# Optimization experiments

Measured on AMD Instinct MI355X. Metric: run time of the kernel, lower is better.

## Reference

```python
import jax, jax.numpy as jnp
import numpy as np

B, N, D_IN, D_OUT, HEADS = 4, 4096, 1024, 1024, 16
D_HEAD = D_OUT // HEADS  # scale_factor in the torch module


def setup_inputs() -> dict:
    key = jax.random.key(0)
    ks = jax.random.split(key, 5)
    x = jax.random.normal(ks[0], (B, N, D_IN), dtype=jnp.float32)
    s_in = 1.0 / np.sqrt(D_IN)
    s_out = 1.0 / np.sqrt(D_OUT)
    Wq = jax.random.normal(ks[1], (D_IN, D_OUT), dtype=jnp.float32) * s_in
    Wk = jax.random.normal(ks[2], (D_IN, D_OUT), dtype=jnp.float32) * s_in
    Wv = jax.random.normal(ks[3], (D_IN, D_OUT), dtype=jnp.float32) * s_in
    Wo = jax.random.normal(ks[4], (D_OUT, D_OUT), dtype=jnp.float32) * s_out
    bo = jnp.zeros((D_OUT,), dtype=jnp.float32)
    return {"x": x, "Wq": Wq, "Wk": Wk, "Wv": Wv, "Wo": Wo, "bo": bo}


def reference(x, Wq, Wk, Wv, Wo, bo):
    # Linear attention (Efficient Attention): softmax(Q, feat) @ (softmax(K, seq)^T @ V)
    q = jax.nn.softmax(jnp.einsum('bni,io->bno', x, Wq), axis=-1)   # [B,N,D] softmax over features
    k = jax.nn.softmax(jnp.einsum('bni,io->bno', x, Wk), axis=-2)   # [B,N,D] softmax over sequence
    v = jnp.einsum('bni,io->bno', x, Wv)                             # [B,N,D]
    scale = 1.0 / np.sqrt(D_HEAD).astype(np.float32)
    # context = K^T V : [B, D, D] -- avoids the [B, N, N] score matrix
    ctx = jnp.einsum('bnd,bne->bde', k, v) * scale
    y = jnp.einsum('bnd,bde->bne', q, ctx) / jnp.float32(D_OUT)      # final per-elem / shape[-1]
    # dropout is identity in eval mode
    return jnp.einsum('bnd,de->bne', y, Wo) + bo
```

## Files before the change

### kernel.cpp

```cpp
#include <hip/hip_runtime.h>

typedef _Float16 half_t;
typedef __attribute__((ext_vector_type(8))) _Float16 half8;
typedef __attribute__((ext_vector_type(4))) _Float16 half4;
typedef __attribute__((ext_vector_type(4))) float f32x4;

#define B_ 4
#define N_ 4096
#define D_ 1024
#define R_ (B_ * N_)

__device__ __forceinline__ void gload_lds16(const half_t* g, half_t* l) {
    __builtin_amdgcn_global_load_lds(
        (const __attribute__((address_space(1))) unsigned int*)g,
        (__attribute__((address_space(3))) unsigned int*)l, 16, 0, 0);
}

__device__ __forceinline__ void wgbar() {
    asm volatile("" ::: "memory");
    __builtin_amdgcn_s_barrier();
    asm volatile("" ::: "memory");
}

template <int EPI, int ZSHIFT, int SWAP>
__global__ __launch_bounds__(512, 2) void gemm256(
    const half_t* __restrict__ A, const half_t* __restrict__ Bt,
    void* __restrict__ Cv, const float* __restrict__ bias,
    int lda, int ldb, int ldc, int K,
    long sA, long sB, long sC, float scale)
{
    __shared__ __align__(16) half_t As[2][2][256 * 32];
    __shared__ __align__(16) half_t Bs[2][2][256 * 32];

    const int t = threadIdx.x;
    const int wave = t >> 6;
    const int lane = t & 63;
    const int l15 = lane & 15;
    const int q = lane >> 4;
    const int wm = wave >> 2;
    const int wn = wave & 3;
    const int m0 = (SWAP ? blockIdx.x : blockIdx.y) * 256;
    const int n0 = (SWAP ? blockIdx.y : blockIdx.x) * 256;
    const long zb = blockIdx.z >> ZSHIFT;
    const int zs = blockIdx.z & ((1 << ZSHIFT) - 1);

    const int c0 = t, c1 = t + 512;
    const int r0 = c0 >> 2, r1 = c1 >> 2;
    const int g0 = ((c0 & 3) ^ ((c0 >> 3) & 3)) * 8;
    const int g1 = ((c1 & 3) ^ ((c1 >> 3) & 3)) * 8;

    const half_t* Ab = A + zb * sA + (long)m0 * lda + zs * K;
    const half_t* Bb = Bt + zb * sB + (long)n0 * ldb + zs * K;
    const long a0 = (long)r0 * lda + g0, a1 = (long)r1 * lda + g1;
    const long b0 = (long)r0 * ldb + g0, b1 = (long)r1 * ldb + g1;

    const int qq = (q ^ ((l15 >> 1) & 3)) * 8;

    f32x4 acc[8][4] = {};
    const int nk2 = K >> 6;

#define STAGE_A(tt, ks) do { const int kb_ = (tt) * 64 + (ks) * 32; \
        gload_lds16(Ab + a0 + kb_, &As[(tt) & 1][ks][c0 * 8]);      \
        gload_lds16(Ab + a1 + kb_, &As[(tt) & 1][ks][c1 * 8]); } while (0)
#define STAGE_B(tt, ks) do { const int kb_ = (tt) * 64 + (ks) * 32; \
        gload_lds16(Bb + b0 + kb_, &Bs[(tt) & 1][ks][c0 * 8]);      \
        gload_lds16(Bb + b1 + kb_, &Bs[(tt) & 1][ks][c1 * 8]); } while (0)
#define LDB4(ksb) _Pragma("unroll") \
    for (int j = 0; j < 4; j++)     \
        bf[j] = *(const half8*)&Bs[cur][ksb][(wn * 64 + j * 16 + l15) * 32 + qq];
#define LDA4(ksb, mh) _Pragma("unroll") \
    for (int i = 0; i < 4; i++)         \
        af[i] = *(const half8*)&As[cur][ksb][(wm * 128 + (mh) * 64 + i * 16 + l15) * 32 + qq];
#define MFMA16(ar) _Pragma("unroll")                    \
    for (int i = 0; i < 4; i++) _Pragma("unroll")       \
        for (int j = 0; j < 4; j++)                     \
            acc[(ar) + i][j] = __builtin_amdgcn_mfma_f32_16x16x32_f16(af[i], bf[j], acc[(ar) + i][j], 0, 0, 0);

    STAGE_A(0, 0); STAGE_B(0, 0); STAGE_A(0, 1); STAGE_B(0, 1);
    if (nk2 > 1) {
        STAGE_A(1, 0); STAGE_B(1, 0); STAGE_B(1, 1);
        asm volatile("s_waitcnt vmcnt(6)" ::: "memory");
    } else {
        asm volatile("s_waitcnt vmcnt(0)" ::: "memory");
    }
    wgbar();

    for (int tt = 0; tt < nk2; ++tt) {
        const int cur = tt & 1;
        half8 af[4], bf[4];
        LDB4(0); LDA4(0, 0);
        if (tt + 1 < nk2) STAGE_A(tt + 1, 1);
        wgbar();
        __builtin_amdgcn_s_setprio(1); MFMA16(0); __builtin_amdgcn_s_setprio(0);
        wgbar();
        LDA4(0, 1);
        if (tt + 2 < nk2) STAGE_B(tt + 2, 0);
        wgbar();
        __builtin_amdgcn_s_setprio(1); MFMA16(4); __builtin_amdgcn_s_setprio(0);
        wgbar();
        LDB4(1); LDA4(1, 0);
        if (tt + 2 < nk2) STAGE_A(tt + 2, 0);
        wgbar();
        __builtin_amdgcn_s_setprio(1); MFMA16(0); __builtin_amdgcn_s_setprio(0);
        wgbar();
        LDA4(1, 1);
        if (tt + 2 < nk2) STAGE_B(tt + 2, 1);
        wgbar();
        __builtin_amdgcn_s_setprio(1); MFMA16(4); __builtin_amdgcn_s_setprio(0);
        if (tt + 2 < nk2) asm volatile("s_waitcnt vmcnt(6)" ::: "memory");
        else              asm volatile("s_waitcnt vmcnt(0)" ::: "memory");
        wgbar();
    }
#undef STAGE_A
#undef STAGE_B
#undef LDB4
#undef LDA4
#undef MFMA16

    if (EPI == 1) {
        half_t* C = (half_t*)Cv + (long)blockIdx.z * sC + (long)m0 * ldc + n0;
#pragma unroll
        for (int a = 0; a < 8; a++) {
            const int rowb = wm * 128 + (a >> 2) * 64 + (a & 3) * 16 + q * 4;
#pragma unroll
            for (int j = 0; j < 4; j++) {
                const int col = wn * 64 + j * 16 + l15;
#pragma unroll
                for (int r = 0; r < 4; r++)
                    C[(long)(rowb + r) * ldc + col] = (half_t)(acc[a][j][r] * scale);
            }
        }
    } else {
        float* C = (float*)Cv + (long)blockIdx.z * sC + (long)m0 * ldc + n0;
#pragma unroll
        for (int a = 0; a < 8; a++) {
            const int rowb = wm * 128 + (a >> 2) * 64 + (a & 3) * 16 + q * 4;
#pragma unroll
            for (int j = 0; j < 4; j++) {
                const int col = wn * 64 + j * 16 + l15;
                const float bv = (EPI == 2) ? bias[n0 + col] : 0.0f;
#pragma unroll
                for (int r = 0; r < 4; r++)
                    C[(long)(rowb + r) * ldc + col] = acc[a][j][r] * scale + bv;
            }
        }
    }
}

__global__ __launch_bounds__(256) void ctx_reduce_h(
    const half_t* __restrict__ P, half_t* __restrict__ ctx)
{
    const long i = ((long)blockIdx.x * 256 + threadIdx.x) * 8;
    const long b = i >> 20;
    const long idx = i & ((1L << 20) - 1);
    const half_t* p = P + (b * 4) * (1L << 20) + idx;
    const half8 s0 = *(const half8*)(p);
    const half8 s1 = *(const half8*)(p + (1L << 20));
    const half8 s2 = *(const half8*)(p + 2 * (1L << 20));
    const half8 s3 = *(const half8*)(p + 3 * (1L << 20));
    half8 o;
#pragma unroll
    for (int j = 0; j < 8; j++)
        o[j] = (half_t)((float)s0[j] + (float)s1[j] + (float)s2[j] + (float)s3[j]);
    *(half8*)(ctx + i) = o;
}

__global__ __launch_bounds__(256) void convert_f32_f16(
    const float* __restrict__ in, half_t* __restrict__ out)
{
    const long i = ((long)blockIdx.x * 256 + threadIdx.x) * 8;
    const float4 a = *(const float4*)(in + i);
    const float4 b = *(const float4*)(in + i + 4);
    half8 o = {(half_t)a.x, (half_t)a.y, (half_t)a.z, (half_t)a.w,
               (half_t)b.x, (half_t)b.y, (half_t)b.z, (half_t)b.w};
    *(half8*)(out + i) = o;
}

__global__ void transpose_w4(const float* __restrict__ W0, const float* __restrict__ W1,
                             const float* __restrict__ W2, const float* __restrict__ W3,
                             half_t* __restrict__ Wt)
{
    __shared__ float tile[32][33];
    const float* W = blockIdx.z == 0 ? W0 : blockIdx.z == 1 ? W1
                   : blockIdx.z == 2 ? W2 : W3;
    half_t* dst = Wt + (size_t)blockIdx.z * 1024 * 1024;
    const int tx = threadIdx.x, ty = threadIdx.y;
    const int bx = blockIdx.x * 32, by = blockIdx.y * 32;
#pragma unroll
    for (int yy = ty; yy < 32; yy += 8)
        tile[yy][tx] = W[(long)(by + yy) * 1024 + bx + tx];
    __syncthreads();
#pragma unroll
    for (int yy = ty; yy < 32; yy += 8)
        dst[(long)(bx + yy) * 1024 + by + tx] = (half_t)tile[tx][yy];
}

__global__ __launch_bounds__(256) void softmax_rows(
    const half_t* __restrict__ L, half_t* __restrict__ Qh)
{
    const int r = blockIdx.x;
    const int t = threadIdx.x;
    const half4 xh = ((const half4*)(L + (long)r * 1024))[t];
    const float x0 = (float)xh[0], x1 = (float)xh[1],
                x2 = (float)xh[2], x3 = (float)xh[3];
    float m = fmaxf(fmaxf(x0, x1), fmaxf(x2, x3));
#pragma unroll
    for (int o = 32; o > 0; o >>= 1) m = fmaxf(m, __shfl_xor(m, o, 64));
    __shared__ float redm[4], reds[4];
    const int wave = t >> 6;
    if ((t & 63) == 0) redm[wave] = m;
    __syncthreads();
    m = fmaxf(fmaxf(redm[0], redm[1]), fmaxf(redm[2], redm[3]));
    const float e0 = __expf(x0 - m), e1 = __expf(x1 - m),
                e2 = __expf(x2 - m), e3 = __expf(x3 - m);
    float s = e0 + e1 + e2 + e3;
#pragma unroll
    for (int o = 32; o > 0; o >>= 1) s += __shfl_xor(s, o, 64);
    if ((t & 63) == 0) reds[wave] = s;
    __syncthreads();
    s = reds[0] + reds[1] + reds[2] + reds[3];
    const float rs = 64.0f / s;
    half4 o4 = {(half_t)(e0 * rs), (half_t)(e1 * rs),
                (half_t)(e2 * rs), (half_t)(e3 * rs)};
    ((half4*)(Qh + (long)r * 1024))[t] = o4;
}

__global__ __launch_bounds__(256) void softmax_seq(
    const half_t* __restrict__ L, half_t* __restrict__ O)
{
    const long r = blockIdx.x;
    const int t = threadIdx.x;
    const half_t* row = L + r * 4096;
    const half8 h0 = *(const half8*)(row + t * 16);
    const half8 h1 = *(const half8*)(row + t * 16 + 8);
    float v[16];
#pragma unroll
    for (int j = 0; j < 8; j++) { v[j] = (float)h0[j]; v[8 + j] = (float)h1[j]; }
    float m = v[0];
#pragma unroll
    for (int j = 1; j < 16; j++) m = fmaxf(m, v[j]);
#pragma unroll
    for (int o = 32; o > 0; o >>= 1) m = fmaxf(m, __shfl_xor(m, o, 64));
    __shared__ float redm[4], reds[4];
    const int wave = t >> 6;
    if ((t & 63) == 0) redm[wave] = m;
    __syncthreads();
    m = fmaxf(fmaxf(redm[0], redm[1]), fmaxf(redm[2], redm[3]));
    float s = 0.0f;
#pragma unroll
    for (int j = 0; j < 16; j++) { v[j] = __expf(v[j] - m); s += v[j]; }
#pragma unroll
    for (int o = 32; o > 0; o >>= 1) s += __shfl_xor(s, o, 64);
    if ((t & 63) == 0) reds[wave] = s;
    __syncthreads();
    s = reds[0] + reds[1] + reds[2] + reds[3];
    const float rs = 64.0f / s;
    half8 o0, o1;
#pragma unroll
    for (int j = 0; j < 8; j++) {
        o0[j] = (half_t)(v[j] * rs);
        o1[j] = (half_t)(v[8 + j] * rs);
    }
    *(half8*)(O + r * 4096 + t * 16) = o0;
    *(half8*)(O + r * 4096 + t * 16 + 8) = o1;
}

extern "C" void kernel_launch(void* const* d_in, const int* in_sizes, int n_in,
                              void* d_out, int out_size, void* d_ws, size_t ws_size,
                              hipStream_t stream)
{
    const float* x  = (const float*)d_in[0];
    const float* Wq = (const float*)d_in[1];
    const float* Wk = (const float*)d_in[2];
    const float* Wv = (const float*)d_in[3];
    const float* Wo = (const float*)d_in[4];
    const float* bo = (const float*)d_in[5];
    float* out = (float*)d_out;

    char* w = (char*)d_ws;
    half_t* Xh  = (half_t*)w;
    half_t* P   = (half_t*)w;
    half_t* L   = (half_t*)(w + ((size_t)R_ * D_ * 2));
    w += (size_t)R_ * D_ * 4;
    half_t* Qh  = (half_t*)w; w += (size_t)R_ * D_ * 2;
    half_t* Kt  = (half_t*)w; w += (size_t)R_ * D_ * 2;
    half_t* Vt  = (half_t*)w; w += (size_t)R_ * D_ * 2;
    half_t* Wt  = (half_t*)w; w += (size_t)4 * D_ * D_ * 2;
    half_t* ctx = (half_t*)w; w += (size_t)B_ * D_ * D_ * 2;
    half_t* Mt  = (half_t*)w; w += (size_t)B_ * D_ * D_ * 2;
    (void)ws_size; (void)in_sizes; (void)n_in; (void)out_size;

    const dim3 blk(256);
    const dim3 blkg(512);
    const long M1 = 1L << 20;

    convert_f32_f16<<<R_ * D_ / (256 * 8), blk, 0, stream>>>(x, Xh);
    transpose_w4<<<dim3(32, 32, 4), dim3(32, 8), 0, stream>>>(Wq, Wk, Wv, Wo, Wt);

    gemm256<1, 0, 1><<<dim3(64, 4, 1), blkg, 0, stream>>>(Xh, Wt, L, nullptr,
        1024, 1024, 1024, 1024, 0, 0, 0, 1.0f);
    softmax_rows<<<R_, blk, 0, stream>>>(L, Qh);

    gemm256<1, 0, 0><<<dim3(16, 4, B_), blkg, 0, stream>>>(Wt + M1, Xh, L, nullptr,
        1024, 1024, 4096, 1024, 0, (long)N_ * D_, (long)D_ * N_, 1.0f);
    softmax_seq<<<B_ * D_, blk, 0, stream>>>(L, Kt);

    gemm256<1, 0, 0><<<dim3(16, 4, B_), blkg, 0, stream>>>(Wt + 2 * M1, Xh, Vt, nullptr,
        1024, 1024, 4096, 1024, 0, (long)N_ * D_, (long)D_ * N_, 1.0f);

    gemm256<1, 2, 1><<<dim3(4, 4, 16), blkg, 0, stream>>>(Kt, Vt, P, nullptr,
        N_, N_, 1024, N_ / 4,
        (long)D_ * N_, (long)D_ * N_, M1, 1.0f);
    ctx_reduce_h<<<2048, blk, 0, stream>>>(P, ctx);

    gemm256<1, 2, 1><<<dim3(4, 4, 16), blkg, 0, stream>>>(Wt + 3 * M1, ctx, P, nullptr,
        1024, 1024, 1024, 256,
        0, M1, M1, 1.0f);
    ctx_reduce_h<<<2048, blk, 0, stream>>>(P, Mt);

    gemm256<2, 0, 1><<<dim3(16, 4, B_), blkg, 0, stream>>>(Qh, Mt, out, bo,
        1024, 1024, 1024, 1024,
        (long)N_ * D_, M1, (long)N_ * D_,
        1.0f / 33554432.0f);
}
```

Before: 389.2 us.

## Simplify GEMM pipeline to 4-buffer K32 stages and fuse K/V projection GEMMs

The GEMM main loop changes from a two-half-K, four-barrier-per-iteration schedule to a simpler four-slot ring of 32-wide K tiles. Two tiles are prefetched ahead, with one barrier per step and all 32 MFMAs issued together. Separately, the K and V projections become one launch with doubled grid height, writing into an interleaved K/V region that softmax_seq and the ctx GEMM index with new strides. This removes a launch and gives more blocks per wave, but the coarser schedule may overlap LDS reads and MFMA less well and raises register pressure (af[8]).

```diff
diff --git a/kernel.cpp b/kernel.cpp
--- a/kernel.cpp
+++ b/kernel.cpp
@@ -29,8 +29,8 @@
     int lda, int ldb, int ldc, int K,
     long sA, long sB, long sC, float scale)
 {
-    __shared__ __align__(16) half_t As[2][2][256 * 32];
-    __shared__ __align__(16) half_t Bs[2][2][256 * 32];
+    __shared__ __align__(16) half_t As[4][256 * 32];
+    __shared__ __align__(16) half_t Bs[4][256 * 32];
 
     const int t = threadIdx.x;
     const int wave = t >> 6;
@@ -57,91 +57,66 @@
     const int qq = (q ^ ((l15 >> 1) & 3)) * 8;
 
     f32x4 acc[8][4] = {};
-    const int nk2 = K >> 6;
-
-#define STAGE_A(tt, ks) do { const int kb_ = (tt) * 64 + (ks) * 32; \
-        gload_lds16(Ab + a0 + kb_, &As[(tt) & 1][ks][c0 * 8]);      \
-        gload_lds16(Ab + a1 + kb_, &As[(tt) & 1][ks][c1 * 8]); } while (0)
-#define STAGE_B(tt, ks) do { const int kb_ = (tt) * 64 + (ks) * 32; \
-        gload_lds16(Bb + b0 + kb_, &Bs[(tt) & 1][ks][c0 * 8]);      \
-        gload_lds16(Bb + b1 + kb_, &Bs[(tt) & 1][ks][c1 * 8]); } while (0)
-#define LDB4(ksb) _Pragma("unroll") \
-    for (int j = 0; j < 4; j++)     \
-        bf[j] = *(const half8*)&Bs[cur][ksb][(wn * 64 + j * 16 + l15) * 32 + qq];
-#define LDA4(ksb, mh) _Pragma("unroll") \
-    for (int i = 0; i < 4; i++)         \
-        af[i] = *(const half8*)&As[cur][ksb][(wm * 128 + (mh) * 64 + i * 16 + l15) * 32 + qq];
-#define MFMA16(ar) _Pragma("unroll")                    \
-    for (int i = 0; i < 4; i++) _Pragma("unroll")       \
-        for (int j = 0; j < 4; j++)                     \
-            acc[(ar) + i][j] = __builtin_amdgcn_mfma_f32_16x16x32_f16(af[i], bf[j], acc[(ar) + i][j], 0, 0, 0);
-
-    STAGE_A(0, 0); STAGE_B(0, 0); STAGE_A(0, 1); STAGE_B(0, 1);
-    if (nk2 > 1) {
-        STAGE_A(1, 0); STAGE_B(1, 0); STAGE_B(1, 1);
-        asm volatile("s_waitcnt vmcnt(6)" ::: "memory");
-    } else {
-        asm volatile("s_waitcnt vmcnt(0)" ::: "memory");
+    const int nk = K >> 5;
+
+#define STAGE(kt) do { const int kb_ = (kt) * 32; const int bf_ = (kt) & 3; \
+        gload_lds16(Ab + a0 + kb_, &As[bf_][c0 * 8]);                       \
+        gload_lds16(Ab + a1 + kb_, &As[bf_][c1 * 8]);                       \
+        gload_lds16(Bb + b0 + kb_, &Bs[bf_][c0 * 8]);                       \
+        gload_lds16(Bb + b1 + kb_, &Bs[bf_][c1 * 8]); } while (0)
+
+    STAGE(0); STAGE(1);
+    asm volatile("s_waitcnt vmcnt(4)" ::: "memory");
+    wgbar();
+
+    for (int kt = 0; kt < nk; ++kt) {
+        const int cb = kt & 3;
+        if (kt + 2 < nk) STAGE(kt + 2);
+        half8 bf[4], af[8];
+#pragma unroll
+        for (int j = 0; j < 4; j++)
+            bf[j] = *(const half8*)&Bs[cb][(wn * 64 + j * 16 + l15) * 32 + qq];
+#pragma unroll
+        for (int i = 0; i < 8; i++)
+            af[i] = *(const half8*)&As[cb][(wm * 128 + i * 16 + l15) * 32 + qq];
+        __builtin_amdgcn_s_setprio(1);
+#pragma unroll
+        for (int i = 0; i < 8; i++)
+#pragma unroll
+            for (int j = 0; j < 4; j++)
+                acc[i][j] = __builtin_amdgcn_mfma_f32_16x16x32_f16(af[i], bf[j], acc[i][j], 0, 0, 0);
+        __builtin_amdgcn_s_setprio(0);
+        if (kt + 2 < nk)      asm volatile("s_waitcnt vmcnt(4)" ::: "memory");
+        else if (kt + 1 < nk) asm volatile("s_waitcnt vmcnt(0)" ::: "memory");
+        if (kt + 1 < nk) wgbar();
     }
-    wgbar();
-
-    for (int tt = 0; tt < nk2; ++tt) {
-        const int cur = tt & 1;
-        half8 af[4], bf[4];
-        LDB4(0); LDA4(0, 0);
-        if (tt + 1 < nk2) STAGE_A(tt + 1, 1);
-        wgbar();
-        __builtin_amdgcn_s_setprio(1); MFMA16(0); __builtin_amdgcn_s_setprio(0);
-        wgbar();
-        LDA4(0, 1);
-        if (tt + 2 < nk2) STAGE_B(tt + 2, 0);
-        wgbar();
-        __builtin_amdgcn_s_setprio(1); MFMA16(4); __builtin_amdgcn_s_setprio(0);
-        wgbar();
-        LDB4(1); LDA4(1, 0);
-        if (tt + 2 < nk2) STAGE_A(tt + 2, 0);
-        wgbar();
-        __builtin_amdgcn_s_setprio(1); MFMA16(0); __builtin_amdgcn_s_setprio(0);
-        wgbar();
-        LDA4(1, 1);
-        if (tt + 2 < nk2) STAGE_B(tt + 2, 1);
-        wgbar();
-        __builtin_amdgcn_s_setprio(1); MFMA16(4); __builtin_amdgcn_s_setprio(0);
-        if (tt + 2 < nk2) asm volatile("s_waitcnt vmcnt(6)" ::: "memory");
-        else              asm volatile("s_waitcnt vmcnt(0)" ::: "memory");
-        wgbar();
-    }
-#undef STAGE_A
-#undef STAGE_B
-#undef LDB4
-#undef LDA4
-#undef MFMA16
+#undef STAGE
 
     if (EPI == 1) {
         half_t* C = (half_t*)Cv + (long)blockIdx.z * sC + (long)m0 * ldc + n0;
 #pragma unroll
-        for (int a = 0; a < 8; a++) {
-            const int rowb = wm * 128 + (a >> 2) * 64 + (a & 3) * 16 + q * 4;
+        for (int i = 0; i < 8; i++) {
+            const int rowb = wm * 128 + i * 16 + q * 4;
 #pragma unroll
             for (int j = 0; j < 4; j++) {
                 const int col = wn * 64 + j * 16 + l15;
 #pragma unroll
                 for (int r = 0; r < 4; r++)
-                    C[(long)(rowb + r) * ldc + col] = (half_t)(acc[a][j][r] * scale);
+                    C[(long)(rowb + r) * ldc + col] = (half_t)(acc[i][j][r] * scale);
             }
         }
     } else {
         float* C = (float*)Cv + (long)blockIdx.z * sC + (long)m0 * ldc + n0;
 #pragma unroll
-        for (int a = 0; a < 8; a++) {
-            const int rowb = wm * 128 + (a >> 2) * 64 + (a & 3) * 16 + q * 4;
+        for (int i = 0; i < 8; i++) {
+            const int rowb = wm * 128 + i * 16 + q * 4;
 #pragma unroll
             for (int j = 0; j < 4; j++) {
                 const int col = wn * 64 + j * 16 + l15;
                 const float bv = (EPI == 2) ? bias[n0 + col] : 0.0f;
 #pragma unroll
                 for (int r = 0; r < 4; r++)
-                    C[(long)(rowb + r) * ldc + col] = acc[a][j][r] * scale + bv;
+                    C[(long)(rowb + r) * ldc + col] = acc[i][j][r] * scale + bv;
             }
         }
     }
@@ -226,11 +201,13 @@
 }
 
 __global__ __launch_bounds__(256) void softmax_seq(
-    const half_t* __restrict__ L, half_t* __restrict__ O)
+    const half_t* __restrict__ KV, half_t* __restrict__ O)
 {
     const long r = blockIdx.x;
+    const long b = r >> 10;
+    const long d = r & 1023;
     const int t = threadIdx.x;
-    const half_t* row = L + r * 4096;
+    const half_t* row = KV + (b * 2048 + d) * 4096;
     const half8 h0 = *(const half8*)(row + t * 16);
     const half8 h1 = *(const half8*)(row + t * 16 + 8);
     float v[16];
@@ -280,11 +257,12 @@
     char* w = (char*)d_ws;
     half_t* Xh  = (half_t*)w;
     half_t* P   = (half_t*)w;
-    half_t* L   = (half_t*)(w + ((size_t)R_ * D_ * 2));
-    w += (size_t)R_ * D_ * 4;
+    w += (size_t)R_ * D_ * 2;
+    half_t* KVreg = (half_t*)w;
+    half_t* Qlog  = KVreg;
+    w += (size_t)B_ * 2048 * 4096 * 2;
     half_t* Qh  = (half_t*)w; w += (size_t)R_ * D_ * 2;
     half_t* Kt  = (half_t*)w; w += (size_t)R_ * D_ * 2;
-    half_t* Vt  = (half_t*)w; w += (size_t)R_ * D_ * 2;
     half_t* Wt  = (half_t*)w; w += (size_t)4 * D_ * D_ * 2;
     half_t* ctx = (half_t*)w; w += (size_t)B_ * D_ * D_ * 2;
     half_t* Mt  = (half_t*)w; w += (size_t)B_ * D_ * D_ * 2;
@@ -297,20 +275,17 @@
     convert_f32_f16<<<R_ * D_ / (256 * 8), blk, 0, stream>>>(x, Xh);
     transpose_w4<<<dim3(32, 32, 4), dim3(32, 8), 0, stream>>>(Wq, Wk, Wv, Wo, Wt);
 
-    gemm256<1, 0, 1><<<dim3(64, 4, 1), blkg, 0, stream>>>(Xh, Wt, L, nullptr,
+    gemm256<1, 0, 1><<<dim3(64, 4, 1), blkg, 0, stream>>>(Xh, Wt, Qlog, nullptr,
         1024, 1024, 1024, 1024, 0, 0, 0, 1.0f);
-    softmax_rows<<<R_, blk, 0, stream>>>(L, Qh);
-
-    gemm256<1, 0, 0><<<dim3(16, 4, B_), blkg, 0, stream>>>(Wt + M1, Xh, L, nullptr,
-        1024, 1024, 4096, 1024, 0, (long)N_ * D_, (long)D_ * N_, 1.0f);
-    softmax_seq<<<B_ * D_, blk, 0, stream>>>(L, Kt);
-
-    gemm256<1, 0, 0><<<dim3(16, 4, B_), blkg, 0, stream>>>(Wt + 2 * M1, Xh, Vt, nullptr,
-        1024, 1024, 4096, 1024, 0, (long)N_ * D_, (long)D_ * N_, 1.0f);
-
-    gemm256<1, 2, 1><<<dim3(4, 4, 16), blkg, 0, stream>>>(Kt, Vt, P, nullptr,
+    softmax_rows<<<R_, blk, 0, stream>>>(Qlog, Qh);
+
+    gemm256<1, 0, 0><<<dim3(16, 8, B_), blkg, 0, stream>>>(Wt + M1, Xh, KVreg, nullptr,
+        1024, 1024, 4096, 1024, 0, (long)N_ * D_, (long)2048 * 4096, 1.0f);
+    softmax_seq<<<B_ * D_, blk, 0, stream>>>(KVreg, Kt);
+
+    gemm256<1, 2, 1><<<dim3(4, 4, 16), blkg, 0, stream>>>(Kt, KVreg + (long)1024 * 4096, P, nullptr,
         N_, N_, 1024, N_ / 4,
-        (long)D_ * N_, (long)D_ * N_, M1, 1.0f);
+        (long)D_ * N_, (long)2048 * 4096, M1, 1.0f);
     ctx_reduce_h<<<2048, blk, 0, stream>>>(P, ctx);
 
     gemm256<1, 2, 1><<<dim3(4, 4, 16), blkg, 0, stream>>>(Wt + 3 * M1, ctx, P, nullptr,
```

Result: slower. 420.1 us (+7.9%).

## Fold Wo into Wv up front and fuse K/V projection GEMMs

Applied to the files above, without the earlier changes.

Precomputes Wv·Wo as a weight-only product before the main pipeline, so the per-batch ctx@Wo GEMM and its reduction disappear. K and V projections are now computed in one GEMM with a doubled grid, writing into an interleaved buffer that softmax_seq and the ctx GEMM index into. The ctx GEMM operand order is swapped to produce the transposed context directly for the final GEMM. This cuts one batched GEMM plus reduction and one launch, at the cost of a small extra weight GEMM and an extra weight conversion, and fp16 rounding of the fused weight may change accuracy.

```diff
diff --git a/kernel.cpp b/kernel.cpp
--- a/kernel.cpp
+++ b/kernel.cpp
@@ -226,11 +226,13 @@
 }
 
 __global__ __launch_bounds__(256) void softmax_seq(
-    const half_t* __restrict__ L, half_t* __restrict__ O)
+    const half_t* __restrict__ KV, half_t* __restrict__ O)
 {
     const long r = blockIdx.x;
+    const long b = r >> 10;
+    const long d = r & 1023;
     const int t = threadIdx.x;
-    const half_t* row = L + r * 4096;
+    const half_t* row = KV + (b * 2048 + d) * 4096;
     const half8 h0 = *(const half8*)(row + t * 16);
     const half8 h1 = *(const half8*)(row + t * 16 + 8);
     float v[16];
@@ -280,14 +282,16 @@
     char* w = (char*)d_ws;
     half_t* Xh  = (half_t*)w;
     half_t* P   = (half_t*)w;
-    half_t* L   = (half_t*)(w + ((size_t)R_ * D_ * 2));
-    w += (size_t)R_ * D_ * 4;
+    w += (size_t)R_ * D_ * 2;
+    half_t* KVreg = (half_t*)w;
+    half_t* Qlog  = KVreg;
+    w += (size_t)B_ * 2048 * 4096 * 2;
     half_t* Qh  = (half_t*)w; w += (size_t)R_ * D_ * 2;
     half_t* Kt  = (half_t*)w; w += (size_t)R_ * D_ * 2;
-    half_t* Vt  = (half_t*)w; w += (size_t)R_ * D_ * 2;
+    half_t* Pw  = Kt;
     half_t* Wt  = (half_t*)w; w += (size_t)4 * D_ * D_ * 2;
-    half_t* ctx = (half_t*)w; w += (size_t)B_ * D_ * D_ * 2;
-    half_t* Mt  = (half_t*)w; w += (size_t)B_ * D_ * D_ * 2;
+    half_t* ctxT = (half_t*)w; w += (size_t)B_ * D_ * D_ * 2;
+    half_t* Wvh = (half_t*)w; w += (size_t)B_ * D_ * D_ * 2;
     (void)ws_size; (void)in_sizes; (void)n_in; (void)out_size;
 
     const dim3 blk(256);
@@ -295,30 +299,27 @@
     const long M1 = 1L << 20;
 
     convert_f32_f16<<<R_ * D_ / (256 * 8), blk, 0, stream>>>(x, Xh);
+    convert_f32_f16<<<512, blk, 0, stream>>>(Wv, Wvh);
     transpose_w4<<<dim3(32, 32, 4), dim3(32, 8), 0, stream>>>(Wq, Wk, Wv, Wo, Wt);
 
-    gemm256<1, 0, 1><<<dim3(64, 4, 1), blkg, 0, stream>>>(Xh, Wt, L, nullptr,
+    gemm256<1, 2, 1><<<dim3(4, 4, 4), blkg, 0, stream>>>(Wt + 3 * M1, Wvh, Pw, nullptr,
+        1024, 1024, 1024, 256, 0, 0, M1, 1.0f);
+    ctx_reduce_h<<<512, blk, 0, stream>>>(Pw, Wt + 2 * M1);
+
+    gemm256<1, 0, 1><<<dim3(64, 4, 1), blkg, 0, stream>>>(Xh, Wt, Qlog, nullptr,
         1024, 1024, 1024, 1024, 0, 0, 0, 1.0f);
-    softmax_rows<<<R_, blk, 0, stream>>>(L, Qh);
-
-    gemm256<1, 0, 0><<<dim3(16, 4, B_), blkg, 0, stream>>>(Wt + M1, Xh, L, nullptr,
-        1024, 1024, 4096, 1024, 0, (long)N_ * D_, (long)D_ * N_, 1.0f);
-    softmax_seq<<<B_ * D_, blk, 0, stream>>>(L, Kt);
-
-    gemm256<1, 0, 0><<<dim3(16, 4, B_), blkg, 0, stream>>>(Wt + 2 * M1, Xh, Vt, nullptr,
-        1024, 1024, 4096, 1024, 0, (long)N_ * D_, (long)D_ * N_, 1.0f);
-
-    gemm256<1, 2, 1><<<dim3(4, 4, 16), blkg, 0, stream>>>(Kt, Vt, P, nullptr,
-        N_, N_, 1024, N_ / 4,
-        (long)D_ * N_, (long)D_ * N_, M1, 1.0f);
-    ctx_reduce_h<<<2048, blk, 0, stream>>>(P, ctx);
-
-    gemm256<1, 2, 1><<<dim3(4, 4, 16), blkg, 0, stream>>>(Wt + 3 * M1, ctx, P, nullptr,
-        1024, 1024, 1024, 256,
-        0, M1, M1, 1.0f);
-    ctx_reduce_h<<<2048, blk, 0, stream>>>(P, Mt);
-
-    gemm256<2, 0, 1><<<dim3(16, 4, B_), blkg, 0, stream>>>(Qh, Mt, out, bo,
+    softmax_rows<<<R_, blk, 0, stream>>>(Qlog, Qh);
+
+    gemm256<1, 0, 0><<<dim3(16, 8, B_), blkg, 0, stream>>>(Wt + M1, Xh, KVreg, nullptr,
+        1024, 1024, 4096, 1024, 0, (long)N_ * D_, (long)2048 * 4096, 1.0f);
+    softmax_seq<<<B_ * D_, blk, 0, stream>>>(KVreg, Kt);
+
+    gemm256<1, 2, 1><<<dim3(4, 4, 16), blkg, 0, stream>>>(KVreg + (long)1024 * 4096, Kt, P, nullptr,
+        4096, 4096, 1024, N_ / 4,
+        (long)2048 * 4096, (long)D_ * N_, M1, 1.0f);
+    ctx_reduce_h<<<2048, blk, 0, stream>>>(P, ctxT);
+
+    gemm256<2, 0, 1><<<dim3(16, 4, B_), blkg, 0, stream>>>(Qh, ctxT, out, bo,
         1024, 1024, 1024, 1024,
         (long)N_ * D_, M1, (long)N_ * D_,
         1.0f / 33554432.0f);
```

Result: no change. 387.6 us (-0.4%).
